# Optimization experiments

Hardware: AMD Instinct MI355X
Metric: run time of the kernel (lower is better)

## Reference

```python
import jax, jax.numpy as jnp
import numpy as np

N_E = 1024    # codebook size
E_DIM = 256   # code dimension
BETA = 0.25   # commitment cost


def setup_inputs() -> dict:
    key = jax.random.key(0)
    k1, k2 = jax.random.split(key)
    z = jax.random.normal(k1, (32, E_DIM, 32, 32), dtype=jnp.float32)
    # embedding init uniform(-1/n_e, 1/n_e) as in the torch module
    e_w = jax.random.uniform(k2, (N_E, E_DIM), jnp.float32, -1.0 / N_E, 1.0 / N_E)
    return {"z": z, "e_w": e_w}


def _vq_forward(z, e_w):
    B, C, H, W = z.shape  # C == E_DIM
    z_flat = jnp.transpose(z, (0, 2, 3, 1)).reshape(-1, C)  # (N, D)
    # squared euclidean distances: ||z||^2 + ||e||^2 - 2 z.e
    d = ((z_flat ** 2).sum(-1, keepdims=True)
         + (e_w ** 2).sum(-1)[None, :]
         - 2.0 * (z_flat @ e_w.T))                          # (N, n_e)
    indices = jnp.argmin(d, axis=1)                          # (N,)
    one_hot = jax.nn.one_hot(indices, N_E, dtype=z.dtype)    # (N, n_e)
    z_q_flat = e_w[indices]                                  # == one_hot @ e_w
    z_q = jnp.transpose(z_q_flat.reshape(B, H, W, C), (0, 3, 1, 2))
    # use_ema=True branch: loss = beta * mse(z_q, sg(z))
    loss = BETA * jnp.mean((z_q - jax.lax.stop_gradient(z)) ** 2)
    # straight-through estimator
    z_q_st = z + jax.lax.stop_gradient(z_q - z)
    avg_probs = one_hot.mean(0)
    perplexity = jnp.exp(-jnp.sum(avg_probs * jnp.log(avg_probs + 1e-10)))
    return loss, z_q_st, perplexity, one_hot, indices


def reference(z, e_w):
    return _vq_forward(z, e_w)
```

## Files before the change

### kernel.cpp

```cpp
#include <hip/hip_runtime.h>
#include <math.h>

#define N_TOK 32768
#define NE    1024
#define DIM   256
#define EPS   8.0e-4f

#define OFF_ZQ   1u
#define OFF_PPL  8388609u
#define OFF_OH   8388610u
#define OFF_IDX  41943042u

#define RS_CAP 4096
#define RS_TOK 16

typedef __attribute__((ext_vector_type(8))) short short8;
typedef __attribute__((ext_vector_type(8))) unsigned short ushort8;
typedef __attribute__((ext_vector_type(4))) float f32x4;
typedef __attribute__((ext_vector_type(2))) float f32x2;

__device__ __forceinline__ unsigned short bf_rne(float f) {
    unsigned u = __float_as_uint(f);
    return (unsigned short)((u + 0x7FFFu + ((u >> 16) & 1u)) >> 16);
}
__device__ __forceinline__ void gload16(const void* g, void* l) {
    __builtin_amdgcn_global_load_lds((const __attribute__((address_space(1))) void*)g,
                                     (__attribute__((address_space(3))) void*)l, 16, 0, 0);
}

__global__ __launch_bounds__(256) void vq_prep(const float* __restrict__ z,
                                               const float* __restrict__ ew,
                                               unsigned short* __restrict__ z1,
                                               unsigned short* __restrict__ e1,
                                               float* __restrict__ zn,
                                               float* __restrict__ en,
                                               float* __restrict__ sse,
                                               int* __restrict__ hist)
{
    __shared__ float zf[64 * 257];
    const int t = threadIdx.x;

    if (blockIdx.x >= 512) {
        if (blockIdx.x == 512 && t == 0) sse[0] = 0.0f;
        const int code = (int)(blockIdx.x - 512) * 256 + t;
        if (hist) hist[code] = 0;
        const float* p = ew + (size_t)code * DIM;
        float s = 0.0f;
        for (int dg = 0; dg < 32; ++dg) {
            ushort8 s1;
#pragma unroll
            for (int j = 0; j < 8; ++j) {
                float v = p[dg * 8 + j];
                s = fmaf(v, v, s);
                s1[j] = bf_rne(v);
            }
            *reinterpret_cast<ushort8*>(e1 + (size_t)code * 256 + dg * 8) = s1;
        }
        en[code] = s;
        return;
    }

    const int img = blockIdx.x >> 4;
    const int hw0 = (blockIdx.x & 15) << 6;
    const float* zb = z + (size_t)img * (DIM * 1024) + hw0;

#pragma unroll
    for (int it = 0; it < 16; ++it) {
        int f = it * 256 + t;
        int c = f >> 4, hw4 = f & 15;
        float4 v = *reinterpret_cast<const float4*>(zb + (size_t)c * 1024 + hw4 * 4);
        zf[(hw4 * 4 + 0) * 257 + c] = v.x;
        zf[(hw4 * 4 + 1) * 257 + c] = v.y;
        zf[(hw4 * 4 + 2) * 257 + c] = v.z;
        zf[(hw4 * 4 + 3) * 257 + c] = v.w;
    }
    __syncthreads();

    if (t < 64) {
        float s = 0.0f;
#pragma unroll 8
        for (int c = 0; c < DIM; ++c) { float v = zf[t * 257 + c]; s = fmaf(v, v, s); }
        zn[img * 1024 + hw0 + t] = s;
    }

#pragma unroll
    for (int it = 0; it < 8; ++it) {
        int f = it * 256 + t;
        int tl = f >> 5, cg = f & 31;
        ushort8 s1;
#pragma unroll
        for (int j = 0; j < 8; ++j)
            s1[j] = (unsigned short)(__float_as_uint(zf[tl * 257 + cg * 8 + j]) >> 16);
        int tok = img * 1024 + hw0 + tl;
        *reinterpret_cast<ushort8*>(z1 + (size_t)tok * 256 + cg * 8) = s1;
    }
}

__global__ __launch_bounds__(256) void vq_argmin_mfma(const unsigned short* __restrict__ z1,
                                                      const unsigned short* __restrict__ e1,
                                                      const float* __restrict__ en,
                                                      unsigned long long* __restrict__ cmu)
{
    __shared__ short lds[2][8192];

    const int t = threadIdx.x;
    const int lane = t & 63, w = t >> 6;
    const int wr = w >> 1, wc = w & 1;
    const int bid = (blockIdx.x & 7) * 256 + (blockIdx.x >> 3);
    const int rb = bid >> 3, cbi = bid & 7;
    const int r0 = rb * 128, c0 = cbi * 128;

    const char* srcp[4];
#pragma unroll
    for (int i = 0; i < 4; ++i) {
        int flat = (w * 4 + i) * 64 + lane;
        int arr = flat >> 9;
        int rr  = (flat & 511) >> 2;
        int sl  = flat & 3;
        int slx = sl ^ ((rr >> 1) & 3);
        srcp[i] = (arr == 0)
            ? (const char*)(z1 + (size_t)(r0 + rr) * 256 + slx * 8)
            : (const char*)(e1 + (size_t)(c0 + rr) * 256 + slx * 8);
    }

    f32x4 acc[4][4];
#pragma unroll
    for (int i = 0; i < 4; ++i)
#pragma unroll
        for (int j = 0; j < 4; ++j) acc[i][j] = (f32x4)0.0f;

#pragma unroll
    for (int i = 0; i < 4; ++i)
        gload16(srcp[i], &lds[0][(w * 4 + i) * 512]);
    __syncthreads();

    int cur = 0;
    for (int kc = 0; kc < 8; ++kc) {
        if (kc < 7) {
            const unsigned kadd = (unsigned)(kc + 1) * 64u;
#pragma unroll
            for (int i = 0; i < 4; ++i)
                gload16(srcp[i] + kadd, &lds[cur ^ 1][(w * 4 + i) * 512]);
        }
        const short* L = &lds[cur][0];
        const short* za = L;
        const short* eb = L + 4096;

        short8 bfr[4];
#pragma unroll
        for (int fn = 0; fn < 4; ++fn) {
            int row = wc * 64 + fn * 16 + (lane & 15);
            int slot = (lane >> 4) ^ ((row >> 1) & 3);
            bfr[fn] = *reinterpret_cast<const short8*>(eb + row * 32 + slot * 8);
        }
#pragma unroll
        for (int fm = 0; fm < 4; ++fm) {
            int row = wr * 64 + fm * 16 + (lane & 15);
            int slot = (lane >> 4) ^ ((row >> 1) & 3);
            short8 a0 = *reinterpret_cast<const short8*>(za + row * 32 + slot * 8);
#pragma unroll
            for (int fn = 0; fn < 4; ++fn)
                acc[fm][fn] = __builtin_amdgcn_mfma_f32_16x16x32_bf16(a0, bfr[fn], acc[fm][fn], 0, 0, 0);
        }
        __syncthreads();
        cur ^= 1;
    }

    float env[4];
#pragma unroll
    for (int fn = 0; fn < 4; ++fn)
        env[fn] = en[c0 + wc * 64 + fn * 16 + (lane & 15)];

    float* sdm = reinterpret_cast<float*>(&lds[0][0]);

#pragma unroll
    for (int fm = 0; fm < 4; ++fm) {
#pragma unroll
        for (int reg = 0; reg < 4; ++reg) {
            int lrow = wr * 64 + fm * 16 + ((lane >> 4) << 2) + reg;
            float bd = 3.0e38f;
#pragma unroll
            for (int fn = 0; fn < 4; ++fn) {
                float dv = env[fn] - 2.0f * acc[fm][fn][reg];
                bd = fminf(bd, dv);
            }
#pragma unroll
            for (int m = 1; m <= 8; m <<= 1)
                bd = fminf(bd, __shfl_xor(bd, m));
            if ((lane & 15) == 0) sdm[wc * 128 + lrow] = bd;
        }
    }
    __syncthreads();
    if (t < 128) sdm[t] = fminf(sdm[t], sdm[128 + t]) + EPS;
    __syncthreads();

#pragma unroll
    for (int fm = 0; fm < 4; ++fm) {
        unsigned long long bl[4][4];
#pragma unroll
        for (int fn = 0; fn < 4; ++fn) {
#pragma unroll
            for (int reg = 0; reg < 4; ++reg) {
                int lrow = wr * 64 + fm * 16 + ((lane >> 4) << 2) + reg;
                float thr = sdm[lrow];
                float dv = env[fn] - 2.0f * acc[fm][fn][reg];
                bl[fn][reg] = __ballot(dv <= thr);
            }
        }
        const int q = lane >> 4;
#pragma unroll
        for (int reg = 0; reg < 4; ++reg) {
            unsigned long long h =
                  ((bl[0][reg] >> (q * 16)) & 0xFFFFull)
                | (((bl[1][reg] >> (q * 16)) & 0xFFFFull) << 16)
                | (((bl[2][reg] >> (q * 16)) & 0xFFFFull) << 32)
                | (((bl[3][reg] >> (q * 16)) & 0xFFFFull) << 48);
            if ((lane & 15) == reg) {
                int row = wr * 64 + fm * 16 + q * 4 + reg;
                cmu[(size_t)(r0 + row) * 16 + cbi * 2 + wc] = h;
            }
        }
    }
}

__global__ __launch_bounds__(256) void vq_rescore(const float* __restrict__ z,
                                                  const float* __restrict__ ew,
                                                  const float* __restrict__ zn,
                                                  const float* __restrict__ en,
                                                  const unsigned long long* __restrict__ cmu,
                                                  float* __restrict__ out_idx,
                                                  float* __restrict__ zq,
                                                  float* __restrict__ sse,
                                                  float* __restrict__ oh,
                                                  int* __restrict__ hist)
{
    __shared__ float zrow[RS_TOK * 260];
    __shared__ unsigned short wl[RS_CAP];
    __shared__ int   wsum[4];
    __shared__ float redf[256];
    __shared__ unsigned long long best[RS_TOK];

    const int t = threadIdx.x, lane = t & 63, w = t >> 6;
    const int bid = (blockIdx.x & 7) * 256 + (blockIdx.x >> 3);
    const int tok0 = bid * RS_TOK;
    const int img = tok0 >> 10, hw0 = tok0 & 1023;

    {
        const float* zc = z + (size_t)img * (DIM * 1024) + (size_t)t * 1024 + hw0;
#pragma unroll
        for (int j = 0; j < 4; ++j) {
            float4 v = *reinterpret_cast<const float4*>(zc + 4 * j);
            zrow[(4 * j + 0) * 260 + t] = v.x;
            zrow[(4 * j + 1) * 260 + t] = v.y;
            zrow[(4 * j + 2) * 260 + t] = v.z;
            zrow[(4 * j + 3) * 260 + t] = v.w;
        }
    }
    if (t < RS_TOK) best[t] = ~0ull;

    unsigned long long v = cmu[(size_t)(tok0 + (t >> 4)) * 16 + (t & 15)];
    int myc = __popcll(v);
    int x = myc;
#pragma unroll
    for (int d = 1; d < 64; d <<= 1) {
        int y = __shfl_up(x, d);
        if (lane >= d) x += y;
    }
    if (lane == 63) wsum[w] = x;
    __syncthreads();
    int woff = 0;
#pragma unroll
    for (int i = 0; i < 4; ++i) woff += (i < w) ? wsum[i] : 0;
    int total = wsum[0] + wsum[1] + wsum[2] + wsum[3];
    int base = woff + x - myc;
    {
        const int wd = t & 15, tk = t >> 4;
        unsigned long long vv = v;
        while (vv) {
            int b = __ffsll((long long)vv) - 1;
            vv &= vv - 1;
            int code = (wd >> 1) * 128 + (wd & 1) * 64 + b;
            if (base < RS_CAP) wl[base] = (unsigned short)((tk << 10) | code);
            ++base;
        }
    }
    __syncthreads();
    if (total > RS_CAP) total = RS_CAP;

    for (int p = t; p < total; p += 256) {
        int e = (int)wl[p];
        int tk = e >> 10, code = e & 1023;
        const float* ep = ew + (size_t)code * DIM;
        const float* zr = &zrow[tk * 260];
        float s = 0.0f;
#pragma unroll 8
        for (int d = 0; d < DIM; d += 4) {
            float4 e4 = *reinterpret_cast<const float4*>(ep + d);
            float4 z4 = *reinterpret_cast<const float4*>(zr + d);
            s = fmaf(z4.x, e4.x, s);
            s = fmaf(z4.y, e4.y, s);
            s = fmaf(z4.z, e4.z, s);
            s = fmaf(z4.w, e4.w, s);
        }
        float dv = (zn[tok0 + tk] + en[code]) - 2.0f * s;
        unsigned long long key = ((unsigned long long)__float_as_uint(dv) << 32) | (unsigned)code;
        atomicMin(&best[tk], key);
    }
    __syncthreads();
    if (t < RS_TOK) {
        int bi = (int)(best[t] & 0x3FFu);
        out_idx[tok0 + t] = (float)bi;
        if (hist) atomicAdd(&hist[bi], 1);
    }

    const int tk2 = t & 15, cg2 = t >> 4;
    const int bidx = (int)(best[tk2] & 0x3FFu);
    const int hwp = hw0 + tk2;
    float part = 0.0f;
    float* zqb = zq + (size_t)img * (DIM * 1024) + hwp;
    const float* ewb = ew + (size_t)bidx * DIM;
#pragma unroll
    for (int i = 0; i < 16; ++i) {
        int c = cg2 * 16 + i;
        float q = ewb[c];
        float zv = zrow[tk2 * 260 + c];
        zqb[(size_t)c << 10] = q;
        float dx = q - zv;
        part = fmaf(dx, dx, part);
    }
    redf[t] = part;
    __syncthreads();
    for (int s2 = 128; s2 > 0; s2 >>= 1) {
        if (t < s2) redf[t] += redf[t + s2];
        __syncthreads();
    }
    if (t == 0) atomicAdd(sse, redf[0]);

    if (oh) {
        const int w2 = t >> 6, lane2 = t & 63;
#pragma unroll
        for (int rr = 0; rr < 4; ++rr) {
            const int row = w2 * 4 + rr;
            const int bi2 = (int)(best[row] & 0x3FFull);
            float* rowp = oh + (size_t)(tok0 + row) * 1024;
#pragma unroll
            for (int j = 0; j < 4; ++j) {
                int i4 = j * 64 + lane2;
                if (i4 < 255) {
                    int k = 2 + i4 * 4;
                    f32x4 vv4;
                    vv4.x = (k     == bi2) ? 1.0f : 0.0f;
                    vv4.y = (k + 1 == bi2) ? 1.0f : 0.0f;
                    vv4.z = (k + 2 == bi2) ? 1.0f : 0.0f;
                    vv4.w = (k + 3 == bi2) ? 1.0f : 0.0f;
                    __builtin_nontemporal_store(vv4, reinterpret_cast<f32x4*>(rowp + k));
                }
            }
            if (lane2 == 0) {
                f32x2 v2; v2.x = (0 == bi2) ? 1.0f : 0.0f; v2.y = (1 == bi2) ? 1.0f : 0.0f;
                __builtin_nontemporal_store(v2, reinterpret_cast<f32x2*>(rowp));
            } else if (lane2 == 1) {
                f32x2 v2; v2.x = (1022 == bi2) ? 1.0f : 0.0f; v2.y = (1023 == bi2) ? 1.0f : 0.0f;
                __builtin_nontemporal_store(v2, reinterpret_cast<f32x2*>(rowp + 1022));
            }
        }
    }
}

__global__ __launch_bounds__(256) void vq_onehot(const float* __restrict__ idxf,
                                                 float* __restrict__ oh)
{
    const unsigned stride = gridDim.x * blockDim.x;
    const unsigned total2 = N_TOK * (NE / 2);
    for (unsigned o2 = blockIdx.x * blockDim.x + threadIdx.x; o2 < total2; o2 += stride) {
        unsigned n = o2 >> 7;
        int k = (int)((o2 & 127u) << 1);
        int idx = (int)idxf[n];
        float2 v;
        v.x = (k == idx) ? 1.0f : 0.0f;
        v.y = (k + 1 == idx) ? 1.0f : 0.0f;
        reinterpret_cast<float2*>(oh)[o2] = v;
    }
}

__global__ __launch_bounds__(1024) void vq_finalize(const int* __restrict__ histg,
                                                    const float* __restrict__ idxf,
                                                    const float* __restrict__ sse,
                                                    float* __restrict__ loss,
                                                    float* __restrict__ ppl)
{
    __shared__ int   hist[NE];
    __shared__ float red[NE];
    const int t = threadIdx.x;
    if (histg) {
        hist[t] = histg[t];
        __syncthreads();
    } else {
        hist[t] = 0;
        __syncthreads();
        const float2* idx2 = reinterpret_cast<const float2*>(idxf);
        for (int i = t; i < N_TOK / 2; i += 1024) {
            float2 v = idx2[i];
            atomicAdd(&hist[(int)v.x], 1);
            atomicAdd(&hist[(int)v.y], 1);
        }
        __syncthreads();
    }
    float p = (float)hist[t] * (1.0f / (float)N_TOK);
    red[t] = p * logf(p + 1e-10f);
    __syncthreads();
    for (int s = 512; s > 0; s >>= 1) {
        if (t < s) red[t] += red[t + s];
        __syncthreads();
    }
    if (t == 0) {
        ppl[0]  = expf(-red[0]);
        loss[0] = 0.25f * sse[0] / (float)(N_TOK * DIM);
    }
}

extern "C" void kernel_launch(void* const* d_in, const int* in_sizes, int n_in,
                              void* d_out, int out_size, void* d_ws, size_t ws_size,
                              hipStream_t stream)
{
    const float* z  = (const float*)d_in[0];
    const float* ew = (const float*)d_in[1];
    float* out = (float*)d_out;

    float* out_idx = out + OFF_IDX;
    float* out_oh  = out + OFF_OH;
    float* out_zq  = out + OFF_ZQ;
    float* out_ppl = out + OFF_PPL;

    const size_t need = 1024u + 33554432u + 524288u + 4194304u + 131072u + 8192u;
    const bool big = ws_size >= need && ws_size >= (size_t)48u * 1024u * 1024u;
    char* base = big ? (char*)d_ws : (char*)out_oh;
    const size_t Z1o = big ? 1024u : 8u;
    const size_t E1o = Z1o + 33554432u;
    const size_t CMo = E1o + 524288u;
    const size_t ZNo = CMo + 4194304u;
    const size_t ENo = ZNo + 131072u;
    const size_t HIo = ENo + 4096u;

    unsigned short* Z1 = (unsigned short*)(base + Z1o);
    unsigned short* E1 = (unsigned short*)(base + E1o);
    unsigned long long* CM = (unsigned long long*)(base + CMo);
    float* ZN = (float*)(base + ZNo);
    float* EN = (float*)(base + ENo);
    int*   HI = big ? (int*)(base + HIo) : nullptr;
    float* SSE = (float*)d_ws;

    vq_prep<<<516, 256, 0, stream>>>(z, ew, Z1, E1, ZN, EN, SSE, HI);
    vq_argmin_mfma<<<2048, 256, 0, stream>>>(Z1, E1, EN, CM);
    vq_rescore<<<2048, 256, 0, stream>>>(z, ew, ZN, EN, CM, out_idx, out_zq, SSE,
                                         big ? out_oh : nullptr, HI);
    if (!big) vq_onehot<<<2048, 256, 0, stream>>>(out_idx, out_oh);
    vq_finalize<<<1, 1024, 0, stream>>>(HI, out_idx, SSE, out, out_ppl);
}
```

Before: 129.8 us.

## Fuse z transpose and bf16 conversion into the MFMA argmin kernel

```diff
diff --git a/kernel.cpp b/kernel.cpp
--- a/kernel.cpp
+++ b/kernel.cpp
@@ -28,78 +28,36 @@
                                      (__attribute__((address_space(3))) void*)l, 16, 0, 0);
 }
 
-__global__ __launch_bounds__(256) void vq_prep(const float* __restrict__ z,
-                                               const float* __restrict__ ew,
-                                               unsigned short* __restrict__ z1,
-                                               unsigned short* __restrict__ e1,
-                                               float* __restrict__ zn,
-                                               float* __restrict__ en,
-                                               float* __restrict__ sse,
-                                               int* __restrict__ hist)
-{
-    __shared__ float zf[64 * 257];
+__global__ __launch_bounds__(256) void vq_eprep(const float* __restrict__ ew,
+                                                unsigned short* __restrict__ e1,
+                                                float* __restrict__ en,
+                                                float* __restrict__ sse,
+                                                int* __restrict__ hist)
+{
     const int t = threadIdx.x;
-
-    if (blockIdx.x >= 512) {
-        if (blockIdx.x == 512 && t == 0) sse[0] = 0.0f;
-        const int code = (int)(blockIdx.x - 512) * 256 + t;
-        if (hist) hist[code] = 0;
-        const float* p = ew + (size_t)code * DIM;
-        float s = 0.0f;
-        for (int dg = 0; dg < 32; ++dg) {
-            ushort8 s1;
-#pragma unroll
-            for (int j = 0; j < 8; ++j) {
-                float v = p[dg * 8 + j];
-                s = fmaf(v, v, s);
-                s1[j] = bf_rne(v);
-            }
-            *reinterpret_cast<ushort8*>(e1 + (size_t)code * 256 + dg * 8) = s1;
-        }
-        en[code] = s;
-        return;
-    }
-
-    const int img = blockIdx.x >> 4;
-    const int hw0 = (blockIdx.x & 15) << 6;
-    const float* zb = z + (size_t)img * (DIM * 1024) + hw0;
-
-#pragma unroll
-    for (int it = 0; it < 16; ++it) {
-        int f = it * 256 + t;
-        int c = f >> 4, hw4 = f & 15;
-        float4 v = *reinterpret_cast<const float4*>(zb + (size_t)c * 1024 + hw4 * 4);
-        zf[(hw4 * 4 + 0) * 257 + c] = v.x;
-        zf[(hw4 * 4 + 1) * 257 + c] = v.y;
-        zf[(hw4 * 4 + 2) * 257 + c] = v.z;
-        zf[(hw4 * 4 + 3) * 257 + c] = v.w;
-    }
-    __syncthreads();
-
-    if (t < 64) {
-        float s = 0.0f;
-#pragma unroll 8
-        for (int c = 0; c < DIM; ++c) { float v = zf[t * 257 + c]; s = fmaf(v, v, s); }
-        zn[img * 1024 + hw0 + t] = s;
-    }
-
-#pragma unroll
-    for (int it = 0; it < 8; ++it) {
-        int f = it * 256 + t;
-        int tl = f >> 5, cg = f & 31;
+    if (blockIdx.x == 0 && t == 0) sse[0] = 0.0f;
+    const int code = (int)blockIdx.x * 256 + t;
+    if (hist) hist[code] = 0;
+    const float* p = ew + (size_t)code * DIM;
+    float s = 0.0f;
+    for (int dg = 0; dg < 32; ++dg) {
         ushort8 s1;
 #pragma unroll
-        for (int j = 0; j < 8; ++j)
-            s1[j] = (unsigned short)(__float_as_uint(zf[tl * 257 + cg * 8 + j]) >> 16);
-        int tok = img * 1024 + hw0 + tl;
-        *reinterpret_cast<ushort8*>(z1 + (size_t)tok * 256 + cg * 8) = s1;
-    }
-}
-
-__global__ __launch_bounds__(256) void vq_argmin_mfma(const unsigned short* __restrict__ z1,
+        for (int j = 0; j < 8; ++j) {
+            float v = p[dg * 8 + j];
+            s = fmaf(v, v, s);
+            s1[j] = bf_rne(v);
+        }
+        *reinterpret_cast<ushort8*>(e1 + (size_t)code * 256 + dg * 8) = s1;
+    }
+    en[code] = s;
+}
+
+__global__ __launch_bounds__(256) void vq_argmin_mfma(const float* __restrict__ z,
                                                       const unsigned short* __restrict__ e1,
                                                       const float* __restrict__ en,
-                                                      unsigned long long* __restrict__ cmu)
+                                                      unsigned long long* __restrict__ cmu,
+                                                      float* __restrict__ zn)
 {
     __shared__ short lds[2][8192];
 
@@ -109,19 +67,25 @@
     const int bid = (blockIdx.x & 7) * 256 + (blockIdx.x >> 3);
     const int rb = bid >> 3, cbi = bid & 7;
     const int r0 = rb * 128, c0 = cbi * 128;
+    const int img = r0 >> 10, hw0 = r0 & 1023;
+
+    const bool zwave = (t < 128);
 
     const char* srcp[4];
-#pragma unroll
-    for (int i = 0; i < 4; ++i) {
-        int flat = (w * 4 + i) * 64 + lane;
-        int arr = flat >> 9;
-        int rr  = (flat & 511) >> 2;
-        int sl  = flat & 3;
-        int slx = sl ^ ((rr >> 1) & 3);
-        srcp[i] = (arr == 0)
-            ? (const char*)(z1 + (size_t)(r0 + rr) * 256 + slx * 8)
-            : (const char*)(e1 + (size_t)(c0 + rr) * 256 + slx * 8);
-    }
+    if (!zwave) {
+#pragma unroll
+        for (int i = 0; i < 4; ++i) {
+            int flat = (w * 4 + i) * 64 + lane;
+            int rr  = (flat & 511) >> 2;
+            int sl  = flat & 3;
+            int slx = sl ^ ((rr >> 1) & 3);
+            srcp[i] = (const char*)(e1 + (size_t)(c0 + rr) * 256 + slx * 8);
+        }
+    }
+
+    const float* zbase = z + (size_t)img * (DIM * 1024) + hw0 + t;
+    const int swz = (t >> 1) & 3;
+    float znacc = 0.0f;
 
     f32x4 acc[4][4];
 #pragma unroll
@@ -129,18 +93,54 @@
 #pragma unroll
         for (int j = 0; j < 4; ++j) acc[i][j] = (f32x4)0.0f;
 
-#pragma unroll
-    for (int i = 0; i < 4; ++i)
-        gload16(srcp[i], &lds[0][(w * 4 + i) * 512]);
+    if (zwave) {
+        ushort8 pk[4];
+#pragma unroll
+        for (int s = 0; s < 4; ++s) {
+#pragma unroll
+            for (int j = 0; j < 8; ++j) {
+                float v = zbase[(size_t)(s * 8 + j) * 1024];
+                znacc = fmaf(v, v, znacc);
+                pk[s][j] = (unsigned short)(__float_as_uint(v) >> 16);
+            }
+        }
+        short* dst = &lds[0][t * 32];
+#pragma unroll
+        for (int s = 0; s < 4; ++s)
+            *reinterpret_cast<ushort8*>(dst + ((s ^ swz) * 8)) = pk[s];
+    } else {
+#pragma unroll
+        for (int i = 0; i < 4; ++i)
+            gload16(srcp[i], &lds[0][(w * 4 + i) * 512]);
+    }
     __syncthreads();
 
     int cur = 0;
     for (int kc = 0; kc < 8; ++kc) {
         if (kc < 7) {
-            const unsigned kadd = (unsigned)(kc + 1) * 64u;
-#pragma unroll
-            for (int i = 0; i < 4; ++i)
-                gload16(srcp[i] + kadd, &lds[cur ^ 1][(w * 4 + i) * 512]);
+            const int kcn = kc + 1;
+            if (zwave) {
+                const float* zc = zbase + (size_t)(kcn * 32) * 1024;
+                ushort8 pk[4];
+#pragma unroll
+                for (int s = 0; s < 4; ++s) {
+#pragma unroll
+                    for (int j = 0; j < 8; ++j) {
+                        float v = zc[(size_t)(s * 8 + j) * 1024];
+                        znacc = fmaf(v, v, znacc);
+                        pk[s][j] = (unsigned short)(__float_as_uint(v) >> 16);
+                    }
+                }
+                short* dst = &lds[cur ^ 1][t * 32];
+#pragma unroll
+                for (int s = 0; s < 4; ++s)
+                    *reinterpret_cast<ushort8*>(dst + ((s ^ swz) * 8)) = pk[s];
+            } else {
+                const unsigned kadd = (unsigned)kcn * 64u;
+#pragma unroll
+                for (int i = 0; i < 4; ++i)
+                    gload16(srcp[i] + kadd, &lds[cur ^ 1][(w * 4 + i) * 512]);
+            }
         }
         const short* L = &lds[cur][0];
         const short* za = L;
@@ -165,6 +165,8 @@
         __syncthreads();
         cur ^= 1;
     }
+
+    if (zwave && cbi == 0) zn[r0 + t] = znacc;
 
     float env[4];
 #pragma unroll
@@ -432,17 +434,15 @@
     float* out_zq  = out + OFF_ZQ;
     float* out_ppl = out + OFF_PPL;
 
-    const size_t need = 1024u + 33554432u + 524288u + 4194304u + 131072u + 8192u;
+    const size_t need = 1024u + 524288u + 4194304u + 131072u + 16384u;
     const bool big = ws_size >= need && ws_size >= (size_t)48u * 1024u * 1024u;
     char* base = big ? (char*)d_ws : (char*)out_oh;
-    const size_t Z1o = big ? 1024u : 8u;
-    const size_t E1o = Z1o + 33554432u;
+    const size_t E1o = big ? 1024u : 8u;
     const size_t CMo = E1o + 524288u;
     const size_t ZNo = CMo + 4194304u;
     const size_t ENo = ZNo + 131072u;
     const size_t HIo = ENo + 4096u;
 
-    unsigned short* Z1 = (unsigned short*)(base + Z1o);
     unsigned short* E1 = (unsigned short*)(base + E1o);
     unsigned long long* CM = (unsigned long long*)(base + CMo);
     float* ZN = (float*)(base + ZNo);
@@ -450,8 +450,8 @@
     int*   HI = big ? (int*)(base + HIo) : nullptr;
     float* SSE = (float*)d_ws;
 
-    vq_prep<<<516, 256, 0, stream>>>(z, ew, Z1, E1, ZN, EN, SSE, HI);
-    vq_argmin_mfma<<<2048, 256, 0, stream>>>(Z1, E1, EN, CM);
+    vq_eprep<<<4, 256, 0, stream>>>(ew, E1, EN, SSE, HI);
+    vq_argmin_mfma<<<2048, 256, 0, stream>>>(z, E1, EN, CM, ZN);
     vq_rescore<<<2048, 256, 0, stream>>>(z, ew, ZN, EN, CM, out_idx, out_zq, SSE,
                                          big ? out_oh : nullptr, HI);
     if (!big) vq_onehot<<<2048, 256, 0, stream>>>(out_idx, out_oh);
```

Measured after the change: 161.2 us. +24.2%, slower.
